# Optimization experiments

Hardware: AMD Instinct MI355X
Metric: run time of the kernel (lower is better)

Reference implementation:

```python
import jax, jax.numpy as jnp
import numpy as np

HIDDEN = 4096
N_EXPERTS = 128
TOP_K = 8
N_GROUP = 1
TOPK_GROUP = 1
ROUTED_SCALING = 1.0
NORM_TOPK_PROB = True


def setup_inputs() -> dict:
    key = jax.random.key(0)
    k1, k2 = jax.random.split(key)
    tokens = 16384  # batch 4 * seq 4096
    hidden_states = jax.random.normal(k1, (tokens, HIDDEN), dtype=jnp.float32)
    # router gate weight (n_routed_experts, hidden_size)
    weight = jax.random.normal(k2, (N_EXPERTS, HIDDEN), dtype=jnp.float32) * 0.02
    # e_score_correction_bias buffer, initialized to zeros in the module
    e_score_correction_bias = jnp.zeros((N_EXPERTS,), dtype=jnp.float32)
    return {"hidden_states": hidden_states, "weight": weight,
            "e_score_correction_bias": e_score_correction_bias}


def _get_topk_indices(scores, bias):
    # scores: [T, E] sigmoid gate scores; bias: [E]
    T = scores.shape[0]
    experts_per_group = N_EXPERTS // N_GROUP
    s = scores + bias[None, :]  # scores_for_choice
    # group score: sum of top-2 corrected scores within each group
    grp = s.reshape(T, N_GROUP, experts_per_group)
    group_scores = jnp.sum(jax.lax.top_k(grp, 2)[0], axis=-1)  # [T, G]
    group_idx = jax.lax.top_k(group_scores, TOPK_GROUP)[1]      # [T, topk_group]
    group_mask = jnp.zeros((T, N_GROUP), dtype=bool).at[
        jnp.arange(T)[:, None], group_idx].set(True)
    score_mask = jnp.repeat(group_mask, experts_per_group, axis=-1)  # [T, E]
    s_masked = jnp.where(score_mask, s, 0.0)
    topk_indices = jax.lax.top_k(s_masked, TOP_K)[1]  # [T, top_k]
    return topk_indices


def reference(hidden_states, weight, e_score_correction_bias):
    x = hidden_states.reshape(-1, HIDDEN).astype(jnp.float32)
    router_logits = x @ weight.astype(jnp.float32).T          # [T, E]
    scores = jax.nn.sigmoid(router_logits)
    topk_indices = _get_topk_indices(scores, e_score_correction_bias)
    topk_weights = jnp.take_along_axis(scores, topk_indices, axis=1)  # [T, top_k]
    if NORM_TOPK_PROB:
        denom = jnp.sum(topk_weights, axis=-1, keepdims=True) + 1e-20
        topk_weights = topk_weights / denom
    topk_weights = topk_weights * ROUTED_SCALING
    return topk_indices, topk_weights
```

## Files before the change

kernel.cpp:

```cpp
#include <hip/hip_runtime.h>
#include <math.h>

#define HIDDEN 4096
#define NEXP   128
#define TOPK   8
#define BT     16
#define CHUNK  64
#define NCHUNK (HIDDEN / CHUNK)
#define SSTR   132
#define PLANE  (NEXP * CHUNK)

typedef int v4i __attribute__((ext_vector_type(4)));

static __device__ __forceinline__ unsigned pack4(int a, int b, int c, int d) {
    return (unsigned)(a & 255) | ((unsigned)(b & 255) << 8) |
           ((unsigned)(c & 255) << 16) | ((unsigned)(d & 255) << 24);
}

static __device__ __forceinline__ void slice5(float val, float scale1,
        int& d0, int& d1, int& d2, int& d3, int& d4) {
    float v = val * scale1;
    float f = __builtin_rintf(v);
    float r = v - f;
    int nh = (int)f;
    int nl = (int)__builtin_rintf(r * 2097152.0f);
    d0 = (nh + 64) >> 7;  d1 = nh - (d0 << 7);
    d2 = (nl + 8192) >> 14;
    int r2 = nl - (d2 << 14);
    d3 = (r2 + 64) >> 7;  d4 = r2 - (d3 << 7);
}

static __device__ __forceinline__ void slice4(float val, float scale1,
        int& d0, int& d1, int& d2, int& d3) {
    float v = val * scale1;
    float f = __builtin_rintf(v);
    float r = v - f;
    int nh = (int)f;
    int nl = (int)__builtin_rintf(r * 16384.0f);
    d0 = (nh + 64) >> 7;  d1 = nh - (d0 << 7);
    d2 = (nl + 64) >> 7;  d3 = nl - (d2 << 7);
}

__global__ __launch_bounds__(256)
void slice_w_kernel(const float* __restrict__ W, signed char* __restrict__ P)
{
    const int t  = blockIdx.x * 256 + threadIdx.x;
    const int e  = t >> 9;
    const int k0 = (t & 511) * 8;
    const float* src = W + (size_t)e * HIDDEN + k0;
    const float4 a = ((const float4*)src)[0];
    const float4 b = ((const float4*)src)[1];

    int p00,p01,p02,p03,p04; slice5(a.x, 32768.0f, p00,p01,p02,p03,p04);
    int p10,p11,p12,p13,p14; slice5(a.y, 32768.0f, p10,p11,p12,p13,p14);
    int p20,p21,p22,p23,p24; slice5(a.z, 32768.0f, p20,p21,p22,p23,p24);
    int p30,p31,p32,p33,p34; slice5(a.w, 32768.0f, p30,p31,p32,p33,p34);
    int p40,p41,p42,p43,p44; slice5(b.x, 32768.0f, p40,p41,p42,p43,p44);
    int p50,p51,p52,p53,p54; slice5(b.y, 32768.0f, p50,p51,p52,p53,p54);
    int p60,p61,p62,p63,p64; slice5(b.z, 32768.0f, p60,p61,p62,p63,p64);
    int p70,p71,p72,p73,p74; slice5(b.w, 32768.0f, p70,p71,p72,p73,p74);

    const int c = k0 >> 6, kin = k0 & 63;
    signed char* base = P + ((size_t)(c * 5) * NEXP + e) * CHUNK + kin;
    uint2 v;
    v.x = pack4(p00,p10,p20,p30); v.y = pack4(p40,p50,p60,p70);
    *(uint2*)(base + 0 * PLANE) = v;
    v.x = pack4(p01,p11,p21,p31); v.y = pack4(p41,p51,p61,p71);
    *(uint2*)(base + 1 * PLANE) = v;
    v.x = pack4(p02,p12,p22,p32); v.y = pack4(p42,p52,p62,p72);
    *(uint2*)(base + 2 * PLANE) = v;
    v.x = pack4(p03,p13,p23,p33); v.y = pack4(p43,p53,p63,p73);
    *(uint2*)(base + 3 * PLANE) = v;
    v.x = pack4(p04,p14,p24,p34); v.y = pack4(p44,p54,p64,p74);
    *(uint2*)(base + 4 * PLANE) = v;
}

static __device__ __forceinline__ void slice_store_x4(char* dst, float4 xa)
{
    int a00,a01,a02,a03; slice4(xa.x, 1024.0f, a00,a01,a02,a03);
    int a10,a11,a12,a13; slice4(xa.y, 1024.0f, a10,a11,a12,a13);
    int a20,a21,a22,a23; slice4(xa.z, 1024.0f, a20,a21,a22,a23);
    int a30,a31,a32,a33; slice4(xa.w, 1024.0f, a30,a31,a32,a33);
    *(unsigned*)(dst + 0 * 1024) = pack4(a00, a10, a20, a30);
    *(unsigned*)(dst + 1 * 1024) = pack4(a01, a11, a21, a31);
    *(unsigned*)(dst + 2 * 1024) = pack4(a02, a12, a22, a32);
    *(unsigned*)(dst + 3 * 1024) = pack4(a03, a13, a23, a33);
}

__global__ __launch_bounds__(256, 4)
void router_kernel(const float* __restrict__ X,
                   const signed char* __restrict__ P,
                   const float* __restrict__ Bias,
                   float* __restrict__ Out, int T)
{
    __shared__ double S[BT * SSTR];
    char* Ast = (char*)S;

    const int tid  = threadIdx.x;
    const int lane = tid & 63;
    const int wave = tid >> 6;
    const int tokBase = blockIdx.x * BT;

    const int sm  = tid & 15;
    const int sk4 = tid >> 4;
    int srow = tokBase + sm; if (srow >= T) srow = T - 1;
    const float* xptr = X + (size_t)srow * HIDDEN + sk4 * 4;
    const int su    = sm * 4 + (sk4 >> 2);
    const int swoff = ((su ^ ((su >> 3) & 7)) << 4) + (sk4 & 3) * 4;

    const int ru0  = (lane & 15) * 4 + (lane >> 4);
    const int rph0 = (ru0 ^ ((ru0 >> 3) & 7)) << 4;

    const int eb0 = wave * 32 + (lane & 15);
    const int koff = (lane >> 4) * 16;
    const size_t boff0 = (size_t)eb0 * CHUNK + koff;
    const size_t boff1 = boff0 + (size_t)16 * CHUNK;

    v4i acc[2][5];
    #pragma unroll
    for (int et = 0; et < 2; et++)
        #pragma unroll
        for (int s = 0; s < 5; s++)
            acc[et][s] = (v4i){0, 0, 0, 0};

    float4 xa = *(const float4*)xptr;
    slice_store_x4(Ast + swoff, xa);
    __syncthreads();

    #pragma unroll 2
    for (int c = 0; c < NCHUNK; c++) {
        const int buf = (c & 1) * 4096;
        if (c + 1 < NCHUNK)
            xa = *(const float4*)(xptr + (c + 1) * CHUNK);

        const char* ap = Ast + buf + rph0;
        const v4i a0 = *(const v4i*)(ap + 0 * 1024);
        const v4i a1 = *(const v4i*)(ap + 1 * 1024);
        const v4i a2 = *(const v4i*)(ap + 2 * 1024);
        const v4i a3 = *(const v4i*)(ap + 3 * 1024);

        const signed char* pc = P + (size_t)(c * 5) * PLANE;
        #pragma unroll
        for (int et = 0; et < 2; et++) {
            const size_t bo = et ? boff1 : boff0;
            const v4i b0 = *(const v4i*)(pc + (size_t)0 * PLANE + bo);
            const v4i b1 = *(const v4i*)(pc + (size_t)1 * PLANE + bo);
            const v4i b2 = *(const v4i*)(pc + (size_t)2 * PLANE + bo);
            const v4i b3 = *(const v4i*)(pc + (size_t)3 * PLANE + bo);
            const v4i b4 = *(const v4i*)(pc + (size_t)4 * PLANE + bo);
            acc[et][0] = __builtin_amdgcn_mfma_i32_16x16x64_i8(a0, b0, acc[et][0], 0, 0, 0);
            acc[et][1] = __builtin_amdgcn_mfma_i32_16x16x64_i8(a0, b1, acc[et][1], 0, 0, 0);
            acc[et][1] = __builtin_amdgcn_mfma_i32_16x16x64_i8(a1, b0, acc[et][1], 0, 0, 0);
            acc[et][2] = __builtin_amdgcn_mfma_i32_16x16x64_i8(a0, b2, acc[et][2], 0, 0, 0);
            acc[et][2] = __builtin_amdgcn_mfma_i32_16x16x64_i8(a1, b1, acc[et][2], 0, 0, 0);
            acc[et][2] = __builtin_amdgcn_mfma_i32_16x16x64_i8(a2, b0, acc[et][2], 0, 0, 0);
            acc[et][3] = __builtin_amdgcn_mfma_i32_16x16x64_i8(a0, b3, acc[et][3], 0, 0, 0);
            acc[et][3] = __builtin_amdgcn_mfma_i32_16x16x64_i8(a1, b2, acc[et][3], 0, 0, 0);
            acc[et][3] = __builtin_amdgcn_mfma_i32_16x16x64_i8(a2, b1, acc[et][3], 0, 0, 0);
            acc[et][3] = __builtin_amdgcn_mfma_i32_16x16x64_i8(a3, b0, acc[et][3], 0, 0, 0);
            acc[et][4] = __builtin_amdgcn_mfma_i32_16x16x64_i8(a0, b4, acc[et][4], 0, 0, 0);
            acc[et][4] = __builtin_amdgcn_mfma_i32_16x16x64_i8(a1, b3, acc[et][4], 0, 0, 0);
            acc[et][4] = __builtin_amdgcn_mfma_i32_16x16x64_i8(a2, b2, acc[et][4], 0, 0, 0);
            acc[et][4] = __builtin_amdgcn_mfma_i32_16x16x64_i8(a3, b1, acc[et][4], 0, 0, 0);
        }

        if (c + 1 < NCHUNK)
            slice_store_x4(Ast + (buf ^ 4096) + swoff, xa);
        __syncthreads();
    }

    {
        const double w0 = 0x1p-11, w1 = 0x1p-18, w2 = 0x1p-25, w3 = 0x1p-32, w4 = 0x1p-39;
        #pragma unroll
        for (int et = 0; et < 2; et++) {
            const int ecol = wave * 32 + et * 16 + (lane & 15);
            const double bias = (double)Bias[ecol];
            #pragma unroll
            for (int r = 0; r < 4; r++) {
                const int trow = (lane >> 4) * 4 + r;
                const double logit = (double)acc[et][0][r] * w0
                                   + (double)acc[et][1][r] * w1
                                   + (double)acc[et][2][r] * w2
                                   + (double)acc[et][3][r] * w3
                                   + (double)acc[et][4][r] * w4;
                S[trow * SSTR + ecol] = 1.0 / (1.0 + exp(-logit)) + bias;
            }
        }
    }
    __syncthreads();

    if (tid < BT * 8) {
        const int tk  = tid >> 3;
        const int j   = tid & 7;
        const int tok = tokBase + tk;
        const double* row = S + tk * SSTR + j * 16;
        double v[16];
        #pragma unroll
        for (int k = 0; k < 16; k++) v[k] = row[k];

        double wts[TOPK]; float idxf[TOPK];
        double wsum = 0.0;
        #pragma unroll
        for (int p = 0; p < TOPK; p++) {
            double best = v[0]; int bi = 0;
            #pragma unroll
            for (int k = 1; k < 16; k++)
                if (v[k] > best) { best = v[k]; bi = k; }
            int be = j * 16 + bi;
            #pragma unroll
            for (int off = 1; off < 8; off <<= 1) {
                double ob = __shfl_xor(best, off, 8);
                int    oe = __shfl_xor(be,   off, 8);
                if (ob > best || (ob == best && oe < be)) { best = ob; be = oe; }
            }
            const bool own = (be >> 4) == j;
            const int  bl  = be & 15;
            #pragma unroll
            for (int k = 0; k < 16; k++)
                if (own && k == bl) v[k] = -1.0e300;
            const double sg = best - (double)Bias[be];
            wts[p]  = sg;
            wsum   += sg;
            idxf[p] = (float)be;
        }
        if (j == 0 && tok < T) {
            const double inv = 1.0 / (wsum + 1e-20);
            float* oi = Out + (size_t)tok * TOPK;
            float* ow = Out + (size_t)T * TOPK + (size_t)tok * TOPK;
            #pragma unroll
            for (int p = 0; p < TOPK; p++) {
                oi[p] = idxf[p];
                ow[p] = (float)(wts[p] * inv);
            }
        }
    }
}

extern "C" void kernel_launch(void* const* d_in, const int* in_sizes, int n_in,
                              void* d_out, int out_size, void* d_ws, size_t ws_size,
                              hipStream_t stream) {
    const float* X    = (const float*)d_in[0];
    const float* W    = (const float*)d_in[1];
    const float* Bias = (const float*)d_in[2];
    float* Out = (float*)d_out;
    const int T = in_sizes[0] / HIDDEN;
    signed char* P = (signed char*)d_ws;

    hipLaunchKernelGGL(slice_w_kernel, dim3(NEXP * 512 / 256), dim3(256), 0, stream, W, P);
    hipLaunchKernelGGL(router_kernel, dim3((T + BT - 1) / BT), dim3(256), 0, stream,
                       X, P, Bias, Out, T);
}
```

Before: 513.3 us.

## Double token tile and slice activations in registers instead of shared memory

The token tile per block grows from 16 to 32, so every wave holds two token sub-tiles and reuses each loaded weight fragment across both, halving weight traffic per token. Each wave now loads and slices its own activations straight into MFMA operand registers, which removes the shared-memory staging buffer and the per-chunk barrier. The cost is a doubled accumulator set and higher register pressure, reflected in the lowered occupancy hint. Activation slicing is also repeated in every wave rather than shared across the block.

New measurement: 508.5 us. About the same (-0.9%).

```diff
diff --git a/kernel.cpp b/kernel.cpp
--- a/kernel.cpp
+++ b/kernel.cpp
@@ -4,7 +4,7 @@
 #define HIDDEN 4096
 #define NEXP   128
 #define TOPK   8
-#define BT     16
+#define BT     32
 #define CHUNK  64
 #define NCHUNK (HIDDEN / CHUNK)
 #define SSTR   132
@@ -75,121 +75,160 @@
     *(uint2*)(base + 4 * PLANE) = v;
 }
 
-static __device__ __forceinline__ void slice_store_x4(char* dst, float4 xa)
+static __device__ __forceinline__ void slice_pack16(
+        const float4 f0, const float4 f1, const float4 f2, const float4 f3,
+        v4i& s0, v4i& s1, v4i& s2, v4i& s3)
 {
-    int a00,a01,a02,a03; slice4(xa.x, 1024.0f, a00,a01,a02,a03);
-    int a10,a11,a12,a13; slice4(xa.y, 1024.0f, a10,a11,a12,a13);
-    int a20,a21,a22,a23; slice4(xa.z, 1024.0f, a20,a21,a22,a23);
-    int a30,a31,a32,a33; slice4(xa.w, 1024.0f, a30,a31,a32,a33);
-    *(unsigned*)(dst + 0 * 1024) = pack4(a00, a10, a20, a30);
-    *(unsigned*)(dst + 1 * 1024) = pack4(a01, a11, a21, a31);
-    *(unsigned*)(dst + 2 * 1024) = pack4(a02, a12, a22, a32);
-    *(unsigned*)(dst + 3 * 1024) = pack4(a03, a13, a23, a33);
-}
-
-__global__ __launch_bounds__(256, 4)
+    unsigned w0[4], w1[4], w2[4], w3[4];
+    {
+        int a0,b0,c0,d0, a1,b1,c1,d1, a2,b2,c2,d2, a3,b3,c3,d3;
+        slice4(f0.x, 1024.0f, a0,a1,a2,a3);
+        slice4(f0.y, 1024.0f, b0,b1,b2,b3);
+        slice4(f0.z, 1024.0f, c0,c1,c2,c3);
+        slice4(f0.w, 1024.0f, d0,d1,d2,d3);
+        w0[0] = pack4(a0,b0,c0,d0); w1[0] = pack4(a1,b1,c1,d1);
+        w2[0] = pack4(a2,b2,c2,d2); w3[0] = pack4(a3,b3,c3,d3);
+    }
+    {
+        int a0,b0,c0,d0, a1,b1,c1,d1, a2,b2,c2,d2, a3,b3,c3,d3;
+        slice4(f1.x, 1024.0f, a0,a1,a2,a3);
+        slice4(f1.y, 1024.0f, b0,b1,b2,b3);
+        slice4(f1.z, 1024.0f, c0,c1,c2,c3);
+        slice4(f1.w, 1024.0f, d0,d1,d2,d3);
+        w0[1] = pack4(a0,b0,c0,d0); w1[1] = pack4(a1,b1,c1,d1);
+        w2[1] = pack4(a2,b2,c2,d2); w3[1] = pack4(a3,b3,c3,d3);
+    }
+    {
+        int a0,b0,c0,d0, a1,b1,c1,d1, a2,b2,c2,d2, a3,b3,c3,d3;
+        slice4(f2.x, 1024.0f, a0,a1,a2,a3);
+        slice4(f2.y, 1024.0f, b0,b1,b2,b3);
+        slice4(f2.z, 1024.0f, c0,c1,c2,c3);
+        slice4(f2.w, 1024.0f, d0,d1,d2,d3);
+        w0[2] = pack4(a0,b0,c0,d0); w1[2] = pack4(a1,b1,c1,d1);
+        w2[2] = pack4(a2,b2,c2,d2); w3[2] = pack4(a3,b3,c3,d3);
+    }
+    {
+        int a0,b0,c0,d0, a1,b1,c1,d1, a2,b2,c2,d2, a3,b3,c3,d3;
+        slice4(f3.x, 1024.0f, a0,a1,a2,a3);
+        slice4(f3.y, 1024.0f, b0,b1,b2,b3);
+        slice4(f3.z, 1024.0f, c0,c1,c2,c3);
+        slice4(f3.w, 1024.0f, d0,d1,d2,d3);
+        w0[3] = pack4(a0,b0,c0,d0); w1[3] = pack4(a1,b1,c1,d1);
+        w2[3] = pack4(a2,b2,c2,d2); w3[3] = pack4(a3,b3,c3,d3);
+    }
+    s0 = (v4i){(int)w0[0], (int)w0[1], (int)w0[2], (int)w0[3]};
+    s1 = (v4i){(int)w1[0], (int)w1[1], (int)w1[2], (int)w1[3]};
+    s2 = (v4i){(int)w2[0], (int)w2[1], (int)w2[2], (int)w2[3]};
+    s3 = (v4i){(int)w3[0], (int)w3[1], (int)w3[2], (int)w3[3]};
+}
+
+__global__ __launch_bounds__(256, 2)
 void router_kernel(const float* __restrict__ X,
                    const signed char* __restrict__ P,
                    const float* __restrict__ Bias,
                    float* __restrict__ Out, int T)
 {
     __shared__ double S[BT * SSTR];
-    char* Ast = (char*)S;
 
     const int tid  = threadIdx.x;
     const int lane = tid & 63;
     const int wave = tid >> 6;
     const int tokBase = blockIdx.x * BT;
 
-    const int sm  = tid & 15;
-    const int sk4 = tid >> 4;
-    int srow = tokBase + sm; if (srow >= T) srow = T - 1;
-    const float* xptr = X + (size_t)srow * HIDDEN + sk4 * 4;
-    const int su    = sm * 4 + (sk4 >> 2);
-    const int swoff = ((su ^ ((su >> 3) & 7)) << 4) + (sk4 & 3) * 4;
-
-    const int ru0  = (lane & 15) * 4 + (lane >> 4);
-    const int rph0 = (ru0 ^ ((ru0 >> 3) & 7)) << 4;
-
-    const int eb0 = wave * 32 + (lane & 15);
-    const int koff = (lane >> 4) * 16;
-    const size_t boff0 = (size_t)eb0 * CHUNK + koff;
+    const int m = lane & 15;
+    const int q = lane >> 4;
+
+    int r0 = tokBase + m;      if (r0 >= T) r0 = T - 1;
+    int r1 = tokBase + 16 + m; if (r1 >= T) r1 = T - 1;
+    const float* xp0 = X + (size_t)r0 * HIDDEN + q * 16;
+    const float* xp1 = X + (size_t)r1 * HIDDEN + q * 16;
+
+    const int eb0 = wave * 32 + m;
+    const size_t boff0 = (size_t)eb0 * CHUNK + q * 16;
     const size_t boff1 = boff0 + (size_t)16 * CHUNK;
 
-    v4i acc[2][5];
+    v4i acc[2][2][5];
     #pragma unroll
-    for (int et = 0; et < 2; et++)
-        #pragma unroll
-        for (int s = 0; s < 5; s++)
-            acc[et][s] = (v4i){0, 0, 0, 0};
-
-    float4 xa = *(const float4*)xptr;
-    slice_store_x4(Ast + swoff, xa);
-    __syncthreads();
+    for (int tt = 0; tt < 2; tt++)
+        #pragma unroll
+        for (int et = 0; et < 2; et++)
+            #pragma unroll
+            for (int s = 0; s < 5; s++)
+                acc[tt][et][s] = (v4i){0, 0, 0, 0};
 
     #pragma unroll 2
     for (int c = 0; c < NCHUNK; c++) {
-        const int buf = (c & 1) * 4096;
-        if (c + 1 < NCHUNK)
-            xa = *(const float4*)(xptr + (c + 1) * CHUNK);
-
-        const char* ap = Ast + buf + rph0;
-        const v4i a0 = *(const v4i*)(ap + 0 * 1024);
-        const v4i a1 = *(const v4i*)(ap + 1 * 1024);
-        const v4i a2 = *(const v4i*)(ap + 2 * 1024);
-        const v4i a3 = *(const v4i*)(ap + 3 * 1024);
+        const float4* x0 = (const float4*)(xp0 + c * CHUNK);
+        const float4* x1 = (const float4*)(xp1 + c * CHUNK);
+        const float4 f00 = x0[0], f01 = x0[1], f02 = x0[2], f03 = x0[3];
+        const float4 f10 = x1[0], f11 = x1[1], f12 = x1[2], f13 = x1[3];
 
         const signed char* pc = P + (size_t)(c * 5) * PLANE;
-        #pragma unroll
-        for (int et = 0; et < 2; et++) {
-            const size_t bo = et ? boff1 : boff0;
-            const v4i b0 = *(const v4i*)(pc + (size_t)0 * PLANE + bo);
-            const v4i b1 = *(const v4i*)(pc + (size_t)1 * PLANE + bo);
-            const v4i b2 = *(const v4i*)(pc + (size_t)2 * PLANE + bo);
-            const v4i b3 = *(const v4i*)(pc + (size_t)3 * PLANE + bo);
-            const v4i b4 = *(const v4i*)(pc + (size_t)4 * PLANE + bo);
-            acc[et][0] = __builtin_amdgcn_mfma_i32_16x16x64_i8(a0, b0, acc[et][0], 0, 0, 0);
-            acc[et][1] = __builtin_amdgcn_mfma_i32_16x16x64_i8(a0, b1, acc[et][1], 0, 0, 0);
-            acc[et][1] = __builtin_amdgcn_mfma_i32_16x16x64_i8(a1, b0, acc[et][1], 0, 0, 0);
-            acc[et][2] = __builtin_amdgcn_mfma_i32_16x16x64_i8(a0, b2, acc[et][2], 0, 0, 0);
-            acc[et][2] = __builtin_amdgcn_mfma_i32_16x16x64_i8(a1, b1, acc[et][2], 0, 0, 0);
-            acc[et][2] = __builtin_amdgcn_mfma_i32_16x16x64_i8(a2, b0, acc[et][2], 0, 0, 0);
-            acc[et][3] = __builtin_amdgcn_mfma_i32_16x16x64_i8(a0, b3, acc[et][3], 0, 0, 0);
-            acc[et][3] = __builtin_amdgcn_mfma_i32_16x16x64_i8(a1, b2, acc[et][3], 0, 0, 0);
-            acc[et][3] = __builtin_amdgcn_mfma_i32_16x16x64_i8(a2, b1, acc[et][3], 0, 0, 0);
-            acc[et][3] = __builtin_amdgcn_mfma_i32_16x16x64_i8(a3, b0, acc[et][3], 0, 0, 0);
-            acc[et][4] = __builtin_amdgcn_mfma_i32_16x16x64_i8(a0, b4, acc[et][4], 0, 0, 0);
-            acc[et][4] = __builtin_amdgcn_mfma_i32_16x16x64_i8(a1, b3, acc[et][4], 0, 0, 0);
-            acc[et][4] = __builtin_amdgcn_mfma_i32_16x16x64_i8(a2, b2, acc[et][4], 0, 0, 0);
-            acc[et][4] = __builtin_amdgcn_mfma_i32_16x16x64_i8(a3, b1, acc[et][4], 0, 0, 0);
-        }
-
-        if (c + 1 < NCHUNK)
-            slice_store_x4(Ast + (buf ^ 4096) + swoff, xa);
-        __syncthreads();
+        v4i b0[5], b1[5];
+        #pragma unroll
+        for (int s = 0; s < 5; s++) {
+            b0[s] = *(const v4i*)(pc + (size_t)s * PLANE + boff0);
+            b1[s] = *(const v4i*)(pc + (size_t)s * PLANE + boff1);
+        }
+
+        v4i a0[4], a1[4];
+        slice_pack16(f00, f01, f02, f03, a0[0], a0[1], a0[2], a0[3]);
+        slice_pack16(f10, f11, f12, f13, a1[0], a1[1], a1[2], a1[3]);
+
+        #pragma unroll
+        for (int tt = 0; tt < 2; tt++) {
+            const v4i A0 = tt ? a1[0] : a0[0];
+            const v4i A1 = tt ? a1[1] : a0[1];
+            const v4i A2 = tt ? a1[2] : a0[2];
+            const v4i A3 = tt ? a1[3] : a0[3];
+            #pragma unroll
+            for (int et = 0; et < 2; et++) {
+                const v4i B0 = et ? b1[0] : b0[0];
+                const v4i B1 = et ? b1[1] : b0[1];
+                const v4i B2 = et ? b1[2] : b0[2];
+                const v4i B3 = et ? b1[3] : b0[3];
+                const v4i B4 = et ? b1[4] : b0[4];
+                acc[tt][et][0] = __builtin_amdgcn_mfma_i32_16x16x64_i8(A0, B0, acc[tt][et][0], 0, 0, 0);
+                acc[tt][et][1] = __builtin_amdgcn_mfma_i32_16x16x64_i8(A0, B1, acc[tt][et][1], 0, 0, 0);
+                acc[tt][et][1] = __builtin_amdgcn_mfma_i32_16x16x64_i8(A1, B0, acc[tt][et][1], 0, 0, 0);
+                acc[tt][et][2] = __builtin_amdgcn_mfma_i32_16x16x64_i8(A0, B2, acc[tt][et][2], 0, 0, 0);
+                acc[tt][et][2] = __builtin_amdgcn_mfma_i32_16x16x64_i8(A1, B1, acc[tt][et][2], 0, 0, 0);
+                acc[tt][et][2] = __builtin_amdgcn_mfma_i32_16x16x64_i8(A2, B0, acc[tt][et][2], 0, 0, 0);
+                acc[tt][et][3] = __builtin_amdgcn_mfma_i32_16x16x64_i8(A0, B3, acc[tt][et][3], 0, 0, 0);
+                acc[tt][et][3] = __builtin_amdgcn_mfma_i32_16x16x64_i8(A1, B2, acc[tt][et][3], 0, 0, 0);
+                acc[tt][et][3] = __builtin_amdgcn_mfma_i32_16x16x64_i8(A2, B1, acc[tt][et][3], 0, 0, 0);
+                acc[tt][et][3] = __builtin_amdgcn_mfma_i32_16x16x64_i8(A3, B0, acc[tt][et][3], 0, 0, 0);
+                acc[tt][et][4] = __builtin_amdgcn_mfma_i32_16x16x64_i8(A0, B4, acc[tt][et][4], 0, 0, 0);
+                acc[tt][et][4] = __builtin_amdgcn_mfma_i32_16x16x64_i8(A1, B3, acc[tt][et][4], 0, 0, 0);
+                acc[tt][et][4] = __builtin_amdgcn_mfma_i32_16x16x64_i8(A2, B2, acc[tt][et][4], 0, 0, 0);
+                acc[tt][et][4] = __builtin_amdgcn_mfma_i32_16x16x64_i8(A3, B1, acc[tt][et][4], 0, 0, 0);
+            }
+        }
     }
 
     {
         const double w0 = 0x1p-11, w1 = 0x1p-18, w2 = 0x1p-25, w3 = 0x1p-32, w4 = 0x1p-39;
         #pragma unroll
-        for (int et = 0; et < 2; et++) {
-            const int ecol = wave * 32 + et * 16 + (lane & 15);
-            const double bias = (double)Bias[ecol];
-            #pragma unroll
-            for (int r = 0; r < 4; r++) {
-                const int trow = (lane >> 4) * 4 + r;
-                const double logit = (double)acc[et][0][r] * w0
-                                   + (double)acc[et][1][r] * w1
-                                   + (double)acc[et][2][r] * w2
-                                   + (double)acc[et][3][r] * w3
-                                   + (double)acc[et][4][r] * w4;
-                S[trow * SSTR + ecol] = 1.0 / (1.0 + exp(-logit)) + bias;
-            }
-        }
+        for (int tt = 0; tt < 2; tt++)
+            #pragma unroll
+            for (int et = 0; et < 2; et++) {
+                const int ecol = wave * 32 + et * 16 + m;
+                const double bias = (double)Bias[ecol];
+                #pragma unroll
+                for (int r = 0; r < 4; r++) {
+                    const int trow = tt * 16 + q * 4 + r;
+                    const double logit = (double)acc[tt][et][0][r] * w0
+                                       + (double)acc[tt][et][1][r] * w1
+                                       + (double)acc[tt][et][2][r] * w2
+                                       + (double)acc[tt][et][3][r] * w3
+                                       + (double)acc[tt][et][4][r] * w4;
+                    S[trow * SSTR + ecol] = 1.0 / (1.0 + exp(-logit)) + bias;
+                }
+            }
     }
     __syncthreads();
 
-    if (tid < BT * 8) {
+    {
         const int tk  = tid >> 3;
         const int j   = tid & 7;
         const int tok = tokBase + tk;
```

## Double token tile, prefetch weight slices across chunks, and prune low-order MFMA products

Applied to the files above, without the earlier changes.

Raises the token tile to 32 per block with 512 threads, so each of 8 waves covers 16 experts across two token sub-tiles. Weight-slice fragments for the next chunk are loaded into registers a chunk ahead, with manual waitcnt and barrier double buffering. The 14-MFMA slice product is cut to 13 by dropping the fifth weight slice plane and reordering the cross terms. This reduces MFMA count and weight-load latency per token, but changes the low-order precision of the logits and raises register pressure.

After: 428.6 us. 1.2x faster.

```diff
diff --git a/kernel.cpp b/kernel.cpp
--- a/kernel.cpp
+++ b/kernel.cpp
@@ -4,7 +4,7 @@
 #define HIDDEN 4096
 #define NEXP   128
 #define TOPK   8
-#define BT     16
+#define BT     32
 #define CHUNK  64
 #define NCHUNK (HIDDEN / CHUNK)
 #define SSTR   132
@@ -81,13 +81,38 @@
     int a10,a11,a12,a13; slice4(xa.y, 1024.0f, a10,a11,a12,a13);
     int a20,a21,a22,a23; slice4(xa.z, 1024.0f, a20,a21,a22,a23);
     int a30,a31,a32,a33; slice4(xa.w, 1024.0f, a30,a31,a32,a33);
-    *(unsigned*)(dst + 0 * 1024) = pack4(a00, a10, a20, a30);
-    *(unsigned*)(dst + 1 * 1024) = pack4(a01, a11, a21, a31);
-    *(unsigned*)(dst + 2 * 1024) = pack4(a02, a12, a22, a32);
-    *(unsigned*)(dst + 3 * 1024) = pack4(a03, a13, a23, a33);
-}
-
-__global__ __launch_bounds__(256, 4)
+    *(unsigned*)(dst + 0 * 2048) = pack4(a00, a10, a20, a30);
+    *(unsigned*)(dst + 1 * 2048) = pack4(a01, a11, a21, a31);
+    *(unsigned*)(dst + 2 * 2048) = pack4(a02, a12, a22, a32);
+    *(unsigned*)(dst + 3 * 2048) = pack4(a03, a13, a23, a33);
+}
+
+#define MFMA13W(BF, BUF)                                                       \
+    {                                                                          \
+        _Pragma("unroll")                                                      \
+        for (int tt = 0; tt < 2; tt++) {                                       \
+            const char* ap = Ast + (BUF) + (tt ? rph1 : rph0);                 \
+            const v4i a0 = *(const v4i*)(ap + 0 * 2048);                       \
+            const v4i a1 = *(const v4i*)(ap + 1 * 2048);                       \
+            const v4i a2 = *(const v4i*)(ap + 2 * 2048);                       \
+            const v4i a3 = *(const v4i*)(ap + 3 * 2048);                       \
+            acc[tt][0] = __builtin_amdgcn_mfma_i32_16x16x64_i8(a0, BF[0], acc[tt][0], 0, 0, 0); \
+            acc[tt][1] = __builtin_amdgcn_mfma_i32_16x16x64_i8(a0, BF[1], acc[tt][1], 0, 0, 0); \
+            acc[tt][2] = __builtin_amdgcn_mfma_i32_16x16x64_i8(a0, BF[2], acc[tt][2], 0, 0, 0); \
+            acc[tt][3] = __builtin_amdgcn_mfma_i32_16x16x64_i8(a0, BF[3], acc[tt][3], 0, 0, 0); \
+            acc[tt][4] = __builtin_amdgcn_mfma_i32_16x16x64_i8(a1, BF[3], acc[tt][4], 0, 0, 0); \
+            acc[tt][1] = __builtin_amdgcn_mfma_i32_16x16x64_i8(a1, BF[0], acc[tt][1], 0, 0, 0); \
+            acc[tt][2] = __builtin_amdgcn_mfma_i32_16x16x64_i8(a1, BF[1], acc[tt][2], 0, 0, 0); \
+            acc[tt][3] = __builtin_amdgcn_mfma_i32_16x16x64_i8(a1, BF[2], acc[tt][3], 0, 0, 0); \
+            acc[tt][4] = __builtin_amdgcn_mfma_i32_16x16x64_i8(a2, BF[2], acc[tt][4], 0, 0, 0); \
+            acc[tt][2] = __builtin_amdgcn_mfma_i32_16x16x64_i8(a2, BF[0], acc[tt][2], 0, 0, 0); \
+            acc[tt][3] = __builtin_amdgcn_mfma_i32_16x16x64_i8(a2, BF[1], acc[tt][3], 0, 0, 0); \
+            acc[tt][4] = __builtin_amdgcn_mfma_i32_16x16x64_i8(a3, BF[1], acc[tt][4], 0, 0, 0); \
+            acc[tt][3] = __builtin_amdgcn_mfma_i32_16x16x64_i8(a3, BF[0], acc[tt][3], 0, 0, 0); \
+        }                                                                      \
+    }
+
+__global__ __launch_bounds__(512, 4)
 void router_kernel(const float* __restrict__ X,
                    const signed char* __restrict__ P,
                    const float* __restrict__ Bias,
@@ -101,88 +126,89 @@
     const int wave = tid >> 6;
     const int tokBase = blockIdx.x * BT;
 
-    const int sm  = tid & 15;
-    const int sk4 = tid >> 4;
+    const int m = lane & 15;
+    const int q = lane >> 4;
+
+    const int sm  = tid & 31;
+    const int sk4 = tid >> 5;
     int srow = tokBase + sm; if (srow >= T) srow = T - 1;
     const float* xptr = X + (size_t)srow * HIDDEN + sk4 * 4;
     const int su    = sm * 4 + (sk4 >> 2);
     const int swoff = ((su ^ ((su >> 3) & 7)) << 4) + (sk4 & 3) * 4;
 
-    const int ru0  = (lane & 15) * 4 + (lane >> 4);
+    const int ru0  = (m     ) * 4 + q;
+    const int ru1  = (m + 16) * 4 + q;
     const int rph0 = (ru0 ^ ((ru0 >> 3) & 7)) << 4;
-
-    const int eb0 = wave * 32 + (lane & 15);
-    const int koff = (lane >> 4) * 16;
-    const size_t boff0 = (size_t)eb0 * CHUNK + koff;
-    const size_t boff1 = boff0 + (size_t)16 * CHUNK;
+    const int rph1 = (ru1 ^ ((ru1 >> 3) & 7)) << 4;
+
+    const size_t boff = (size_t)(wave * 16 + m) * CHUNK + (size_t)q * 16;
 
     v4i acc[2][5];
     #pragma unroll
-    for (int et = 0; et < 2; et++)
+    for (int tt = 0; tt < 2; tt++)
         #pragma unroll
         for (int s = 0; s < 5; s++)
-            acc[et][s] = (v4i){0, 0, 0, 0};
-
-    float4 xa = *(const float4*)xptr;
-    slice_store_x4(Ast + swoff, xa);
-    __syncthreads();
-
-    #pragma unroll 2
-    for (int c = 0; c < NCHUNK; c++) {
-        const int buf = (c & 1) * 4096;
-        if (c + 1 < NCHUNK)
-            xa = *(const float4*)(xptr + (c + 1) * CHUNK);
-
-        const char* ap = Ast + buf + rph0;
-        const v4i a0 = *(const v4i*)(ap + 0 * 1024);
-        const v4i a1 = *(const v4i*)(ap + 1 * 1024);
-        const v4i a2 = *(const v4i*)(ap + 2 * 1024);
-        const v4i a3 = *(const v4i*)(ap + 3 * 1024);
-
-        const signed char* pc = P + (size_t)(c * 5) * PLANE;
-        #pragma unroll
-        for (int et = 0; et < 2; et++) {
-            const size_t bo = et ? boff1 : boff0;
-            const v4i b0 = *(const v4i*)(pc + (size_t)0 * PLANE + bo);
-            const v4i b1 = *(const v4i*)(pc + (size_t)1 * PLANE + bo);
-            const v4i b2 = *(const v4i*)(pc + (size_t)2 * PLANE + bo);
-            const v4i b3 = *(const v4i*)(pc + (size_t)3 * PLANE + bo);
-            const v4i b4 = *(const v4i*)(pc + (size_t)4 * PLANE + bo);
-            acc[et][0] = __builtin_amdgcn_mfma_i32_16x16x64_i8(a0, b0, acc[et][0], 0, 0, 0);
-            acc[et][1] = __builtin_amdgcn_mfma_i32_16x16x64_i8(a0, b1, acc[et][1], 0, 0, 0);
-            acc[et][1] = __builtin_amdgcn_mfma_i32_16x16x64_i8(a1, b0, acc[et][1], 0, 0, 0);
-            acc[et][2] = __builtin_amdgcn_mfma_i32_16x16x64_i8(a0, b2, acc[et][2], 0, 0, 0);
-            acc[et][2] = __builtin_amdgcn_mfma_i32_16x16x64_i8(a1, b1, acc[et][2], 0, 0, 0);
-            acc[et][2] = __builtin_amdgcn_mfma_i32_16x16x64_i8(a2, b0, acc[et][2], 0, 0, 0);
-            acc[et][3] = __builtin_amdgcn_mfma_i32_16x16x64_i8(a0, b3, acc[et][3], 0, 0, 0);
-            acc[et][3] = __builtin_amdgcn_mfma_i32_16x16x64_i8(a1, b2, acc[et][3], 0, 0, 0);
-            acc[et][3] = __builtin_amdgcn_mfma_i32_16x16x64_i8(a2, b1, acc[et][3], 0, 0, 0);
-            acc[et][3] = __builtin_amdgcn_mfma_i32_16x16x64_i8(a3, b0, acc[et][3], 0, 0, 0);
-            acc[et][4] = __builtin_amdgcn_mfma_i32_16x16x64_i8(a0, b4, acc[et][4], 0, 0, 0);
-            acc[et][4] = __builtin_amdgcn_mfma_i32_16x16x64_i8(a1, b3, acc[et][4], 0, 0, 0);
-            acc[et][4] = __builtin_amdgcn_mfma_i32_16x16x64_i8(a2, b2, acc[et][4], 0, 0, 0);
-            acc[et][4] = __builtin_amdgcn_mfma_i32_16x16x64_i8(a3, b1, acc[et][4], 0, 0, 0);
-        }
-
-        if (c + 1 < NCHUNK)
-            slice_store_x4(Ast + (buf ^ 4096) + swoff, xa);
-        __syncthreads();
+            acc[tt][s] = (v4i){0, 0, 0, 0};
+
+    {
+        float4 xa = *(const float4*)xptr;
+        slice_store_x4(Ast + swoff, xa);
+    }
+    v4i bfE[4], bfO[4];
+    #pragma unroll
+    for (int s = 0; s < 4; s++)
+        bfE[s] = *(const v4i*)(P + (size_t)s * PLANE + boff);
+    float4 xo = *(const float4*)(xptr + CHUNK);
+
+    asm volatile("s_waitcnt lgkmcnt(0)" ::: "memory");
+    __builtin_amdgcn_s_barrier();
+
+    float4 xe;
+    #pragma unroll 1
+    for (int c = 0; c < NCHUNK; c += 2) {
+        {
+            const signed char* pn = P + (size_t)((c + 1) * 5) * PLANE;
+            #pragma unroll
+            for (int s = 0; s < 4; s++)
+                bfO[s] = *(const v4i*)(pn + (size_t)s * PLANE + boff);
+            xe = *(const float4*)(xptr + ((c + 2) & (NCHUNK - 1)) * CHUNK);
+
+            MFMA13W(bfE, 0)
+
+            slice_store_x4(Ast + 8192 + swoff, xo);
+            asm volatile("s_waitcnt lgkmcnt(0)" ::: "memory");
+            __builtin_amdgcn_s_barrier();
+        }
+        {
+            const signed char* pn = P + (size_t)(((c + 2) & (NCHUNK - 1)) * 5) * PLANE;
+            #pragma unroll
+            for (int s = 0; s < 4; s++)
+                bfE[s] = *(const v4i*)(pn + (size_t)s * PLANE + boff);
+            xo = *(const float4*)(xptr + ((c + 3) & (NCHUNK - 1)) * CHUNK);
+
+            MFMA13W(bfO, 8192)
+
+            if (c + 2 < NCHUNK)
+                slice_store_x4(Ast + swoff, xe);
+            asm volatile("s_waitcnt lgkmcnt(0)" ::: "memory");
+            __builtin_amdgcn_s_barrier();
+        }
     }
 
     {
         const double w0 = 0x1p-11, w1 = 0x1p-18, w2 = 0x1p-25, w3 = 0x1p-32, w4 = 0x1p-39;
-        #pragma unroll
-        for (int et = 0; et < 2; et++) {
-            const int ecol = wave * 32 + et * 16 + (lane & 15);
-            const double bias = (double)Bias[ecol];
+        const int ecol = wave * 16 + m;
+        const double bias = (double)Bias[ecol];
+        #pragma unroll
+        for (int tt = 0; tt < 2; tt++) {
             #pragma unroll
             for (int r = 0; r < 4; r++) {
-                const int trow = (lane >> 4) * 4 + r;
-                const double logit = (double)acc[et][0][r] * w0
-                                   + (double)acc[et][1][r] * w1
-                                   + (double)acc[et][2][r] * w2
-                                   + (double)acc[et][3][r] * w3
-                                   + (double)acc[et][4][r] * w4;
+                const int trow = tt * 16 + q * 4 + r;
+                const double logit = (double)acc[tt][0][r] * w0
+                                   + (double)acc[tt][1][r] * w1
+                                   + (double)acc[tt][2][r] * w2
+                                   + (double)acc[tt][3][r] * w3
+                                   + (double)acc[tt][4][r] * w4;
                 S[trow * SSTR + ecol] = 1.0 / (1.0 + exp(-logit)) + bias;
             }
         }
@@ -247,6 +273,6 @@
     signed char* P = (signed char*)d_ws;
 
     hipLaunchKernelGGL(slice_w_kernel, dim3(NEXP * 512 / 256), dim3(256), 0, stream, W, P);
-    hipLaunchKernelGGL(router_kernel, dim3((T + BT - 1) / BT), dim3(256), 0, stream,
+    hipLaunchKernelGGL(router_kernel, dim3((T + BT - 1) / BT), dim3(512), 0, stream,
                        X, P, Bias, Out, T);
 }
```
